# Performance work log

Hardware: AMD Instinct MI355X
Metric: run time of the kernel (lower is better)

## Reference

```python
import jax, jax.numpy as jnp
import numpy as np


def _edt(mask_zero):
    """Exact 2D Euclidean distance transform: distance of every pixel to the
    nearest True pixel in mask_zero (matches scipy.ndimage.distance_transform_edt
    applied to the one-hot map, where background pixels are zeros).
    mask_zero: [B, C, H, W] bool, True where the one-hot map is 0.
    Returns float32 [B, C, H, W].
    """
    B, C, H, W = mask_zero.shape
    BIG = jnp.float32(H + W)  # larger than any in-image 1D distance

    # Phase 1: 1D distance to nearest zero along axis H (forward + backward scans)
    def step(d, m):  # d,m: [B, C, W]
        d = jnp.where(m, 0.0, d + 1.0)
        return d, d

    m_rows = jnp.moveaxis(mask_zero, 2, 0)  # [H, B, C, W]
    init = jnp.full((B, C, W), BIG, dtype=jnp.float32)
    _, g_f = jax.lax.scan(step, init, m_rows)
    _, g_b = jax.lax.scan(step, init, m_rows[::-1])
    g = jnp.minimum(g_f, g_b[::-1])          # [H, B, C, W]
    g = jnp.moveaxis(g, 0, 2)                # [B, C, H, W]

    # Phase 2: exact combine along axis W: d2[.., i, j] = min_k g[.., i, k]^2 + (j-k)^2
    j = jnp.arange(W, dtype=jnp.float32)
    sq = (j[:, None] - j[None, :]) ** 2      # [W(j), W(k)]
    d2 = jnp.min(g[..., None, :] ** 2 + sq, axis=-1)  # [B, C, H, W]
    return jnp.sqrt(d2)


def _rrwmap(y_, num_classes):
    labels = y_[:, 0]  # [B, H, W]
    # one-hot channel c is zero where label != c
    mask_zero = labels[:, None, :, :] != jnp.arange(num_classes)[None, :, None, None]
    d = _edt(mask_zero)                                  # [B, C, H, W]
    maxd = jnp.max(d, axis=(2, 3), keepdims=True)        # per (b, c) max
    rrw = -(d / (maxd + 1e-15))
    return jnp.where(rrw == 0.0, 1.0, rrw)


def setup_inputs() -> dict:
    key = jax.random.key(0)
    k1, k2 = jax.random.split(key)
    B, C, H, W = 2, 4, 256, 256
    x = jax.random.normal(k1, (B, C, H, W), dtype=jnp.float32)
    y_ = jax.random.randint(k2, (B, 1, H, W), 0, C, dtype=jnp.int64)
    return {"x": x, "y_": y_}


def reference(x, y_):
    C = x.shape[1]
    rrw = _rrwmap(y_, C)
    p = jax.nn.softmax(x, axis=1)
    return jnp.mean(p * rrw)
```

## Files before the change

### kernel.cpp

```cpp
#include <hip/hip_runtime.h>

#define B_ 2
#define C_ 4
#define H_ 256
#define W_ 256
constexpr int BC    = B_ * C_;
constexpr int HW    = H_ * W_;
constexpr int NROWS = BC * H_;
constexpr int NTOT  = B_ * C_ * HW;
constexpr float BIGF = (float)(H_ + W_);

__global__ __launch_bounds__(256) void rows_kernel(
    const int* __restrict__ lab, const float* __restrict__ x,
    float* __restrict__ pa, float* __restrict__ ps, float* __restrict__ pm) {
    const int r  = blockIdx.x;
    const int bc = r >> 8;
    const int i  = r & (H_ - 1);
    const int b  = bc >> 2;
    const int c  = bc & (C_ - 1);
    const int j  = threadIdx.x;
    const int* lcol = lab + b * HW + j;

    float up;
    {
        int k = 0;
        for (;;) {
            const int row = i - k;
            if (row < 0) { up = BIGF + (float)(i + 1); break; }
            if (lcol[row * W_] != c) { up = (float)k; break; }
            ++k;
        }
    }
    float dn;
    {
        int k = 0;
        for (;;) {
            const int row = i + k;
            if (row >= H_) { dn = BIGF + (float)(H_ - i); break; }
            if (lcol[row * W_] != c) { dn = (float)k; break; }
            ++k;
        }
    }
    const float g = fminf(up, dn);

    __shared__ float g2s[W_];
    const float g2 = g * g;
    g2s[j] = g2;
    __syncthreads();

    float best = g2;
    if (best > 0.0f) {
        for (int dj = 1; dj < W_; ++dj) {
            const float dd = (float)(dj * dj);
            if (dd >= best) break;
            const int l = j - dj, rr = j + dj;
            if (l >= 0)  best = fminf(best, g2s[l] + dd);
            if (rr < W_) best = fminf(best, g2s[rr] + dd);
        }
    }

    const float* xp = x + b * C_ * HW + i * W_ + j;
    const float x0 = xp[0 * HW], x1 = xp[1 * HW], x2 = xp[2 * HW], x3 = xp[3 * HW];
    const float mx = fmaxf(fmaxf(x0, x1), fmaxf(x2, x3));
    const float e0 = __expf(x0 - mx), e1 = __expf(x1 - mx);
    const float e2 = __expf(x2 - mx), e3 = __expf(x3 - mx);
    const float ec = (c == 0) ? e0 : (c == 1) ? e1 : (c == 2) ? e2 : e3;
    const float p  = ec / (e0 + e1 + e2 + e3);

    float va = (best == 0.0f) ? p : 0.0f;
    float vs = (best == 0.0f) ? 0.0f : p * sqrtf(best);
    float vm = best;

    #pragma unroll
    for (int off = 32; off; off >>= 1) {
        va += __shfl_down(va, off, 64);
        vs += __shfl_down(vs, off, 64);
        vm = fmaxf(vm, __shfl_down(vm, off, 64));
    }
    __shared__ float sa[4], ss[4], sm[4];
    const int lane = j & 63, wid = j >> 6;
    if (lane == 0) { sa[wid] = va; ss[wid] = vs; sm[wid] = vm; }
    __syncthreads();
    if (j == 0) {
        pa[r] = sa[0] + sa[1] + sa[2] + sa[3];
        ps[r] = ss[0] + ss[1] + ss[2] + ss[3];
        pm[r] = fmaxf(fmaxf(sm[0], sm[1]), fmaxf(sm[2], sm[3]));
    }
}

__global__ __launch_bounds__(256) void final_kernel(
    const float* __restrict__ pa, const float* __restrict__ ps,
    const float* __restrict__ pm, float* __restrict__ out) {
    const int t = threadIdx.x;
    __shared__ float sa[4], ss[4], sm[4];
    float total = 0.0f;
    for (int bc = 0; bc < BC; ++bc) {
        const int r = bc * H_ + t;
        float va = pa[r], vs = ps[r], vm = pm[r];
        #pragma unroll
        for (int off = 32; off; off >>= 1) {
            va += __shfl_down(va, off, 64);
            vs += __shfl_down(vs, off, 64);
            vm = fmaxf(vm, __shfl_down(vm, off, 64));
        }
        const int lane = t & 63, wid = t >> 6;
        __syncthreads();
        if (lane == 0) { sa[wid] = va; ss[wid] = vs; sm[wid] = vm; }
        __syncthreads();
        if (t == 0) {
            const float A = sa[0] + sa[1] + sa[2] + sa[3];
            const float S = ss[0] + ss[1] + ss[2] + ss[3];
            const float M = fmaxf(fmaxf(sm[0], sm[1]), fmaxf(sm[2], sm[3]));
            total += A - S / (sqrtf(M) + 1e-15f);
        }
    }
    if (t == 0) out[0] = total / (float)NTOT;
}

extern "C" void kernel_launch(void* const* d_in, const int* in_sizes, int n_in,
                              void* d_out, int out_size, void* d_ws, size_t ws_size,
                              hipStream_t stream) {
    const float* x = (const float*)d_in[0];
    const int*   y = (const int*)d_in[1];
    float* out = (float*)d_out;

    float* pa = (float*)d_ws;
    float* ps = pa + NROWS;
    float* pm = ps + NROWS;

    rows_kernel<<<NROWS, W_, 0, stream>>>(y, x, pa, ps, pm);
    final_kernel<<<1, 256, 0, stream>>>(pa, ps, pm, out);
}
```

Measured before the change: 66.60 us.

## Compute all classes per pixel in one pass exploiting one-hot label structure

```diff
diff --git a/kernel.cpp b/kernel.cpp
--- a/kernel.cpp
+++ b/kernel.cpp
@@ -6,112 +6,156 @@
 #define W_ 256
 constexpr int BC    = B_ * C_;
 constexpr int HW    = H_ * W_;
-constexpr int NROWS = BC * H_;
+constexpr int NROWS = B_ * H_;
 constexpr int NTOT  = B_ * C_ * HW;
 constexpr float BIGF = (float)(H_ + W_);
 
 __global__ __launch_bounds__(256) void rows_kernel(
     const int* __restrict__ lab, const float* __restrict__ x,
-    float* __restrict__ pa, float* __restrict__ ps, float* __restrict__ pm) {
-    const int r  = blockIdx.x;
-    const int bc = r >> 8;
-    const int i  = r & (H_ - 1);
-    const int b  = bc >> 2;
-    const int c  = bc & (C_ - 1);
-    const int j  = threadIdx.x;
+    float* __restrict__ ps4, float* __restrict__ pm4, float* __restrict__ pa) {
+    const int r = blockIdx.x;
+    const int b = r >> 8;
+    const int i = r & (H_ - 1);
+    const int j = threadIdx.x;
+
+    const int* lrow = lab + b * HW + i * W_;
+    const int  c    = lrow[j];
+
+    const float* xp = x + b * C_ * HW + i * W_ + j;
+    const float x0 = xp[0 * HW], x1 = xp[1 * HW], x2 = xp[2 * HW], x3 = xp[3 * HW];
+
     const int* lcol = lab + b * HW + j;
-
-    float up;
-    {
-        int k = 0;
-        for (;;) {
-            const int row = i - k;
-            if (row < 0) { up = BIGF + (float)(i + 1); break; }
-            if (lcol[row * W_] != c) { up = (float)k; break; }
-            ++k;
+    float gu = -1.0f, gd = -1.0f;
+    for (int k = 1; gu < 0.0f || gd < 0.0f; ++k) {
+        if (gu < 0.0f) {
+            const int rr = i - k;
+            if (rr < 0) gu = BIGF + (float)(i + 1);
+            else if (lcol[rr * W_] != c) gu = (float)k;
+        }
+        if (gd < 0.0f) {
+            const int rr = i + k;
+            if (rr >= H_) gd = BIGF + (float)(H_ - i);
+            else if (lcol[rr * W_] != c) gd = (float)k;
         }
     }
-    float dn;
-    {
-        int k = 0;
-        for (;;) {
-            const int row = i + k;
-            if (row >= H_) { dn = BIGF + (float)(H_ - i); break; }
-            if (lcol[row * W_] != c) { dn = (float)k; break; }
-            ++k;
-        }
-    }
-    const float g = fminf(up, dn);
+    const float g = fminf(gu, gd);
 
+    __shared__ int   ls[W_];
     __shared__ float g2s[W_];
-    const float g2 = g * g;
-    g2s[j] = g2;
+    ls[j]  = c;
+    g2s[j] = g * g;
     __syncthreads();
 
-    float best = g2;
-    if (best > 0.0f) {
-        for (int dj = 1; dj < W_; ++dj) {
-            const float dd = (float)(dj * dj);
-            if (dd >= best) break;
-            const int l = j - dj, rr = j + dj;
-            if (l >= 0)  best = fminf(best, g2s[l] + dd);
-            if (rr < W_) best = fminf(best, g2s[rr] + dd);
+    float best = g * g;
+    for (int dj = 1; dj < W_; ++dj) {
+        const float dd = (float)(dj * dj);
+        if (dd >= best) break;
+        const int l = j - dj, rr = j + dj;
+        if (l >= 0) {
+            const float v = (ls[l] == c ? g2s[l] : 0.0f) + dd;
+            best = fminf(best, v);
+        }
+        if (rr < W_) {
+            const float v = (ls[rr] == c ? g2s[rr] : 0.0f) + dd;
+            best = fminf(best, v);
         }
     }
 
-    const float* xp = x + b * C_ * HW + i * W_ + j;
-    const float x0 = xp[0 * HW], x1 = xp[1 * HW], x2 = xp[2 * HW], x3 = xp[3 * HW];
     const float mx = fmaxf(fmaxf(x0, x1), fmaxf(x2, x3));
     const float e0 = __expf(x0 - mx), e1 = __expf(x1 - mx);
     const float e2 = __expf(x2 - mx), e3 = __expf(x3 - mx);
+    const float s  = e0 + e1 + e2 + e3;
     const float ec = (c == 0) ? e0 : (c == 1) ? e1 : (c == 2) ? e2 : e3;
-    const float p  = ec / (e0 + e1 + e2 + e3);
+    const float pc = ec / s;
 
-    float va = (best == 0.0f) ? p : 0.0f;
-    float vs = (best == 0.0f) ? 0.0f : p * sqrtf(best);
-    float vm = best;
+    float va = (s - ec) / s;
+    const float psv = pc * sqrtf(best);
+    float s0 = (c == 0) ? psv : 0.0f, s1 = (c == 1) ? psv : 0.0f;
+    float s2 = (c == 2) ? psv : 0.0f, s3 = (c == 3) ? psv : 0.0f;
+    float m0 = (c == 0) ? best : 0.0f, m1 = (c == 1) ? best : 0.0f;
+    float m2 = (c == 2) ? best : 0.0f, m3 = (c == 3) ? best : 0.0f;
 
     #pragma unroll
     for (int off = 32; off; off >>= 1) {
         va += __shfl_down(va, off, 64);
-        vs += __shfl_down(vs, off, 64);
-        vm = fmaxf(vm, __shfl_down(vm, off, 64));
+        s0 += __shfl_down(s0, off, 64);
+        s1 += __shfl_down(s1, off, 64);
+        s2 += __shfl_down(s2, off, 64);
+        s3 += __shfl_down(s3, off, 64);
+        m0 = fmaxf(m0, __shfl_down(m0, off, 64));
+        m1 = fmaxf(m1, __shfl_down(m1, off, 64));
+        m2 = fmaxf(m2, __shfl_down(m2, off, 64));
+        m3 = fmaxf(m3, __shfl_down(m3, off, 64));
     }
-    __shared__ float sa[4], ss[4], sm[4];
+    __shared__ float lred[4][9];
     const int lane = j & 63, wid = j >> 6;
-    if (lane == 0) { sa[wid] = va; ss[wid] = vs; sm[wid] = vm; }
+    if (lane == 0) {
+        lred[wid][0] = va;
+        lred[wid][1] = s0; lred[wid][2] = s1; lred[wid][3] = s2; lred[wid][4] = s3;
+        lred[wid][5] = m0; lred[wid][6] = m1; lred[wid][7] = m2; lred[wid][8] = m3;
+    }
     __syncthreads();
     if (j == 0) {
-        pa[r] = sa[0] + sa[1] + sa[2] + sa[3];
-        ps[r] = ss[0] + ss[1] + ss[2] + ss[3];
-        pm[r] = fmaxf(fmaxf(sm[0], sm[1]), fmaxf(sm[2], sm[3]));
+        float A = 0.0f, S0 = 0.0f, S1 = 0.0f, S2 = 0.0f, S3 = 0.0f;
+        float M0 = 0.0f, M1 = 0.0f, M2 = 0.0f, M3 = 0.0f;
+        #pragma unroll
+        for (int w = 0; w < 4; ++w) {
+            A  += lred[w][0];
+            S0 += lred[w][1]; S1 += lred[w][2]; S2 += lred[w][3]; S3 += lred[w][4];
+            M0 = fmaxf(M0, lred[w][5]); M1 = fmaxf(M1, lred[w][6]);
+            M2 = fmaxf(M2, lred[w][7]); M3 = fmaxf(M3, lred[w][8]);
+        }
+        ((float4*)ps4)[r] = make_float4(S0, S1, S2, S3);
+        ((float4*)pm4)[r] = make_float4(M0, M1, M2, M3);
+        pa[r] = A;
     }
 }
 
 __global__ __launch_bounds__(256) void final_kernel(
-    const float* __restrict__ pa, const float* __restrict__ ps,
-    const float* __restrict__ pm, float* __restrict__ out) {
+    const float4* __restrict__ ps4, const float4* __restrict__ pm4,
+    const float* __restrict__ pa, float* __restrict__ out) {
     const int t = threadIdx.x;
-    __shared__ float sa[4], ss[4], sm[4];
+    const int lane = t & 63, wid = t >> 6;
+    __shared__ float lred[4][9];
     float total = 0.0f;
-    for (int bc = 0; bc < BC; ++bc) {
-        const int r = bc * H_ + t;
-        float va = pa[r], vs = ps[r], vm = pm[r];
+    for (int b = 0; b < B_; ++b) {
+        const int r = b * H_ + t;
+        float4 s4 = ps4[r];
+        float4 m4 = pm4[r];
+        float  a  = pa[r];
         #pragma unroll
         for (int off = 32; off; off >>= 1) {
-            va += __shfl_down(va, off, 64);
-            vs += __shfl_down(vs, off, 64);
-            vm = fmaxf(vm, __shfl_down(vm, off, 64));
+            a    += __shfl_down(a, off, 64);
+            s4.x += __shfl_down(s4.x, off, 64);
+            s4.y += __shfl_down(s4.y, off, 64);
+            s4.z += __shfl_down(s4.z, off, 64);
+            s4.w += __shfl_down(s4.w, off, 64);
+            m4.x = fmaxf(m4.x, __shfl_down(m4.x, off, 64));
+            m4.y = fmaxf(m4.y, __shfl_down(m4.y, off, 64));
+            m4.z = fmaxf(m4.z, __shfl_down(m4.z, off, 64));
+            m4.w = fmaxf(m4.w, __shfl_down(m4.w, off, 64));
         }
-        const int lane = t & 63, wid = t >> 6;
         __syncthreads();
-        if (lane == 0) { sa[wid] = va; ss[wid] = vs; sm[wid] = vm; }
+        if (lane == 0) {
+            lred[wid][0] = a;
+            lred[wid][1] = s4.x; lred[wid][2] = s4.y;
+            lred[wid][3] = s4.z; lred[wid][4] = s4.w;
+            lred[wid][5] = m4.x; lred[wid][6] = m4.y;
+            lred[wid][7] = m4.z; lred[wid][8] = m4.w;
+        }
         __syncthreads();
         if (t == 0) {
-            const float A = sa[0] + sa[1] + sa[2] + sa[3];
-            const float S = ss[0] + ss[1] + ss[2] + ss[3];
-            const float M = fmaxf(fmaxf(sm[0], sm[1]), fmaxf(sm[2], sm[3]));
-            total += A - S / (sqrtf(M) + 1e-15f);
+            float A = 0.0f, S0 = 0.0f, S1 = 0.0f, S2 = 0.0f, S3 = 0.0f;
+            float M0 = 0.0f, M1 = 0.0f, M2 = 0.0f, M3 = 0.0f;
+            #pragma unroll
+            for (int w = 0; w < 4; ++w) {
+                A  += lred[w][0];
+                S0 += lred[w][1]; S1 += lred[w][2]; S2 += lred[w][3]; S3 += lred[w][4];
+                M0 = fmaxf(M0, lred[w][5]); M1 = fmaxf(M1, lred[w][6]);
+                M2 = fmaxf(M2, lred[w][7]); M3 = fmaxf(M3, lred[w][8]);
+            }
+            total += A - S0 / (sqrtf(M0) + 1e-15f) - S1 / (sqrtf(M1) + 1e-15f)
+                       - S2 / (sqrtf(M2) + 1e-15f) - S3 / (sqrtf(M3) + 1e-15f);
         }
     }
     if (t == 0) out[0] = total / (float)NTOT;
@@ -124,10 +168,10 @@
     const int*   y = (const int*)d_in[1];
     float* out = (float*)d_out;
 
-    float* pa = (float*)d_ws;
-    float* ps = pa + NROWS;
-    float* pm = ps + NROWS;
+    float* ps4 = (float*)d_ws;
+    float* pm4 = ps4 + NROWS * 4;
+    float* pa  = pm4 + NROWS * 4;
 
-    rows_kernel<<<NROWS, W_, 0, stream>>>(y, x, pa, ps, pm);
-    final_kernel<<<1, 256, 0, stream>>>(pa, ps, pm, out);
+    rows_kernel<<<NROWS, W_, 0, stream>>>(y, x, ps4, pm4, pa);
+    final_kernel<<<1, 256, 0, stream>>>((const float4*)ps4, (const float4*)pm4, pa, out);
 }
```

After: 63.86 us. -4.1%, faster.
